# Performance work log

Measured on AMD Instinct MI355X. Metric: run time of the kernel, lower is better.

The kernel has to match this reference:

```python
import jax, jax.numpy as jnp
import numpy as np

EPSILON = 0.01
NITER = 5
EPS_MASS = 1e-9
EPS_LSE = 1e-6


def setup_inputs() -> dict:
    key = jax.random.key(0)
    k1, k2 = jax.random.split(key)
    y = jax.random.uniform(k1, (16, 1, 48, 48), dtype=jnp.float32)
    y_target = jax.random.uniform(k2, (16, 1, 48, 48), dtype=jnp.float32)
    return {"y": y, "y_target": y_target}


def _grid_points(h, w):
    # torch.linspace(0, h-1, h)/h == arange(h)/h
    yg = jnp.arange(h, dtype=jnp.float32) / h
    xg = jnp.arange(w, dtype=jnp.float32) / w
    gy, gx = jnp.meshgrid(yg, xg, indexing="ij")
    return jnp.stack([gy.reshape(-1), gx.reshape(-1)], axis=-1)  # [n, 2]


def reference(y, y_target):
    b, c, h, w = y_target.shape
    g = _grid_points(h, w)                     # [n, 2], same for x and y measures
    # cost_matrix with p=2: sum_k |g_i - g_j|^2 ; grids identical across batch,
    # so compute once as [n, n] and broadcast.
    C = ((g[:, None, :] - g[None, :, :]) ** 2).sum(-1)  # [n, n]

    mass_x = jnp.clip(y.reshape(b, -1), 0.0, 1e9) + EPS_MASS
    mass_y = jnp.clip(y_target.reshape(b, -1), 0.0, 1e9) + EPS_MASS
    mu = mass_x / mass_x.sum(-1, keepdims=True)   # [b, n]
    nu = mass_y / mass_y.sum(-1, keepdims=True)   # [b, n]
    log_mu = jnp.log(mu)
    log_nu = jnp.log(nu)

    def M(u, v):
        # (-C_ij + u_i + v_j) / epsilon, shape [b, n, n]
        return (-C[None, :, :] + u[:, :, None] + v[:, None, :]) / EPSILON

    def lse(A):
        # faithful to original: log(sum(exp(A), axis=2) + 1e-6) (non-shifted)
        return jnp.log(jnp.exp(A).sum(2) + EPS_LSE)

    u = jnp.zeros_like(mu)
    v = jnp.zeros_like(nu)
    for _ in range(NITER):
        u = EPSILON * (log_mu - lse(M(u, v))) + u
        v = EPSILON * (log_nu - lse(jnp.swapaxes(M(u, v), 1, 2))) + v

    pi = jnp.exp(M(u, v))                      # [b, n, n] transport plan
    cost = (pi * C[None, :, :]).sum((1, 2))    # [b]
    return jnp.mean(cost)
```

## Files before the change

kernel.cpp:

```cpp
#include <hip/hip_runtime.h>


#define TPB 576
#define STRIDE 72
#define POISON 0xAAAAAAAAu

typedef __attribute__((ext_vector_type(8))) short short8;
typedef __attribute__((ext_vector_type(4))) short short4v;
typedef __attribute__((ext_vector_type(4))) float f32x4;

__device__ __forceinline__ void splitb(float x, short& hi, short& lo) {
    union { float f; unsigned u; } a, h;
    a.f = x;
    h.u = a.u & 0xffff0000u;
    hi  = (short)(h.u >> 16);
    union { float f; unsigned u; } l;
    l.f = x - h.f;
    lo  = (short)(l.u >> 16);
}

__device__ __forceinline__ short bf16rne(float x) {
    union { float f; unsigned u; } a;
    a.f = x;
    unsigned r = a.u + 0x7fffu + ((a.u >> 16) & 1u);
    return (short)(r >> 16);
}

__device__ __forceinline__ f32x4 mm16(short8 a, short8 b, f32x4 c) {
    return __builtin_amdgcn_mfma_f32_16x16x32_bf16(a, b, c, 0, 0, 0);
}

__global__ __launch_bounds__(TPB) void sinkhorn_kernel(const float* __restrict__ y,
                                                       const float* __restrict__ yt,
                                                       unsigned* __restrict__ parts,
                                                       unsigned* __restrict__ ctr,
                                                       float* __restrict__ out)
{
    __shared__ __align__(16) short sW [48 * STRIDE];
    __shared__ __align__(16) short sP [48 * STRIDE];
    __shared__ __align__(16) short sP2[48 * STRIDE];
    __shared__ float red[32];

    const int t    = threadIdx.x;
    const int b    = blockIdx.x;
    const int lane = t & 63;
    const int wid  = t >> 6;
    const int tr   = wid / 3;
    const int tc   = wid - tr * 3;
    const int n15  = lane & 15;
    const int quad = lane >> 4;
    const int kq   = quad * 8;
    const int r0   = tr * 16 + quad * 4;
    const int c    = tc * 16 + n15;
    const int aBase  = (tr * 16 + n15) * STRIDE;
    const int stBase = c * STRIDE + r0;

    const f32x4 y4  = *(const f32x4*)(y  + b * 2304 + c * 48 + r0);
    const f32x4 yt4 = *(const f32x4*)(yt + b * 2304 + c * 48 + r0);

    short8 Tr0, Tr1;
    short8 Th0, Th1, Tl0, Tl1;
    short8 Dh0, Dh1, Dl0, Dl1;
    {
        const float gm = (float)c / 48.0f;
#pragma unroll
        for (int kk = 0; kk < 8; ++kk) {
            int k0 = kq + kk;
            float d = gm - (float)k0 / 48.0f;
            float dsq = d * d;
            float e = __expf(-100.0f * dsq);
            short h, l;
            Tr0[kk] = bf16rne(e);
            splitb(e, h, l);        Th0[kk] = h; Tl0[kk] = l;
            splitb(e * dsq, h, l);  Dh0[kk] = h; Dl0[kk] = l;
            int k1 = k0 + 32;
            if (k1 < 48) {
                float d1 = gm - (float)k1 / 48.0f;
                float q1 = d1 * d1;
                float e1 = __expf(-100.0f * q1);
                Tr1[kk] = bf16rne(e1);
                splitb(e1, h, l);       Th1[kk] = h; Tl1[kk] = l;
                splitb(e1 * q1, h, l);  Dh1[kk] = h; Dl1[kk] = l;
            } else {
                Tr1[kk] = 0;
                Th1[kk] = 0; Tl1[kk] = 0; Dh1[kk] = 0; Dl1[kk] = 0;
            }
        }
    }

    if (t < 432) {
        const short8 zer  = {0, 0, 0, 0, 0, 0, 0, 0};
        const short  o    = (short)0x3F80;
        const short8 ones = {o, o, o, o, o, o, o, o};
        int ccol = t % 9;
        ((short8*)sW)[t] = (ccol < 6) ? ones : zer;
        if (ccol >= 6) {
            ((short8*)sP )[t] = zer;
            ((short8*)sP2)[t] = zer;
        }
    }

    float mx[4], my[4];
#pragma unroll
    for (int rg = 0; rg < 4; ++rg) {
        mx[rg] = fminf(fmaxf(y4[rg],  0.f), 1e9f) + 1e-9f;
        my[rg] = fminf(fmaxf(yt4[rg], 0.f), 1e9f) + 1e-9f;
    }
    float sx = mx[0] + mx[1] + mx[2] + mx[3];
    float sy = my[0] + my[1] + my[2] + my[3];
#pragma unroll
    for (int off = 32; off > 0; off >>= 1) {
        sx += __shfl_down(sx, off);
        sy += __shfl_down(sy, off);
    }
    if (lane == 0) { red[wid] = sx; red[16 + wid] = sy; }
    __syncthreads();
    float ax = 0.f, ay = 0.f;
#pragma unroll
    for (int w = 0; w < TPB / 64; ++w) { ax += red[w]; ay += red[16 + w]; }
    const float rsx = 1.0f / ax, rsy = 1.0f / ay;

    float mu_[4], nu_[4];
#pragma unroll
    for (int q = 0; q < 4; ++q) { mu_[q] = mx[q] * rsx; nu_[q] = my[q] * rsy; }

    float wu_[4] = {1, 1, 1, 1}, wv_[4] = {1, 1, 1, 1};

    const f32x4 zz = {0.f, 0.f, 0.f, 0.f};

    for (int half = 0; half < 10; ++half) {
        {
            short8 a0 = *(const short8*)(sW + aBase + kq);
            short8 a1 = *(const short8*)(sW + aBase + kq + 32);
            f32x4 x  = mm16(a0, Tr0, zz);
            f32x4 yy = mm16(a1, Tr1, zz);
            f32x4 p = x + yy;
            short4v pk;
#pragma unroll
            for (int rg = 0; rg < 4; ++rg) pk[rg] = bf16rne(p[rg]);
            *(short4v*)(sP + stBase) = pk;
        }
        __syncthreads();
        {
            short8 a0 = *(const short8*)(sP + aBase + kq);
            short8 a1 = *(const short8*)(sP + aBase + kq + 32);
            f32x4 x  = mm16(a0, Tr0, zz);
            f32x4 yy = mm16(a1, Tr1, zz);
            f32x4 S = x + yy;
            float* wc       = ((half & 1) == 0) ? wu_ : wv_;
            const float* m_ = ((half & 1) == 0) ? mu_ : nu_;
            short4v wk;
#pragma unroll
            for (int q = 0; q < 4; ++q) {
                wc[q] = wc[q] * m_[q] / (wc[q] * S[q] + 1e-6f);
                wk[q] = bf16rne(wc[q]);
            }
            *(short4v*)(sW + stBase) = wk;
        }
        __syncthreads();
    }

    {
        short8 a0 = *(const short8*)(sW + aBase + kq);
        short8 a1 = *(const short8*)(sW + aBase + kq + 32);
        f32x4 x1 = mm16(a0, Th0, zz), w1 = mm16(a1, Th1, zz);
        x1 = mm16(a0, Tl0, x1);  w1 = mm16(a1, Tl1, w1);
        f32x4 p1 = x1 + w1;
        f32x4 x2 = mm16(a0, Dh0, zz), w2 = mm16(a1, Dh1, zz);
        x2 = mm16(a0, Dl0, x2);  w2 = mm16(a1, Dl1, w2);
        f32x4 p2 = x2 + w2;
        short4v k1, k2;
#pragma unroll
        for (int rg = 0; rg < 4; ++rg) { k1[rg] = bf16rne(p1[rg]); k2[rg] = bf16rne(p2[rg]); }
        *(short4v*)(sP  + stBase) = k1;
        *(short4v*)(sP2 + stBase) = k2;
    }
    __syncthreads();
    float local;
    {
        short8 a0 = *(const short8*)(sP  + aBase + kq);
        short8 a1 = *(const short8*)(sP  + aBase + kq + 32);
        short8 c0 = *(const short8*)(sP2 + aBase + kq);
        short8 c1 = *(const short8*)(sP2 + aBase + kq + 32);
        f32x4 x  = mm16(a0, Dh0, zz), yy = mm16(a1, Dh1, zz);
        x  = mm16(a0, Dl0, x);   yy = mm16(a1, Dl1, yy);
        x  = mm16(c0, Th0, x);   yy = mm16(c1, Th1, yy);
        x  = mm16(c0, Tl0, x);   yy = mm16(c1, Tl1, yy);
        f32x4 G = x + yy;
        local = wu_[0] * G[0] + wu_[1] * G[1] + wu_[2] * G[2] + wu_[3] * G[3];
    }
#pragma unroll
    for (int off = 32; off > 0; off >>= 1) local += __shfl_down(local, off);
    if (lane == 0) red[wid] = local;
    __syncthreads();

    if (t == 0) {
        float total = 0.f;
#pragma unroll
        for (int w = 0; w < TPB / 64; ++w) total += red[w];
        union { float f; unsigned u; } pu; pu.f = total;
        __hip_atomic_store(&parts[b], pu.u, __ATOMIC_RELEASE,
                           __HIP_MEMORY_SCOPE_AGENT);
        unsigned old = __hip_atomic_fetch_add(ctr, 1u, __ATOMIC_ACQ_REL,
                                              __HIP_MEMORY_SCOPE_AGENT);
        if (old == POISON + 15u) {
            float tot = 0.f;
#pragma unroll
            for (int i = 0; i < 16; ++i) {
                union { unsigned u; float f; } q;
                q.u = __hip_atomic_load(&parts[i], __ATOMIC_RELAXED,
                                        __HIP_MEMORY_SCOPE_AGENT);
                tot += q.f;
            }
            out[0] = tot * (1.0f / 16.0f);
        }
    }
}

extern "C" void kernel_launch(void* const* d_in, const int* in_sizes, int n_in,
                              void* d_out, int out_size, void* d_ws, size_t ws_size,
                              hipStream_t stream)
{
    (void)in_sizes; (void)n_in; (void)ws_size; (void)out_size;
    const float* y  = (const float*)d_in[0];
    const float* yt = (const float*)d_in[1];
    unsigned* parts = (unsigned*)d_ws;
    unsigned* ctr   = (unsigned*)d_ws + 16;
    float*    out   = (float*)d_out;

    sinkhorn_kernel<<<16, TPB, 0, stream>>>(y, yt, parts, ctr, out);
}
```

Baseline: 67.83 us.

## Collapse each batch to a single wavefront with register-shuffle operand exchange

Replaces the 9-wavefront block, which used shared memory and barriers between each separable Gaussian matmul, with one 64-thread wavefront per batch item. Each lane holds a 3x3 grid of MFMA tiles in registers and rebuilds the B operands with cross-lane shuffles, so no LDS or __syncthreads is needed. The kernel matrix is built from shuffles of a 1-D Gaussian table, and the final cost drops the hi/lo bf16 split in favour of single bf16 rounding. The aim is to remove barrier and LDS round-trip latency, in exchange for serial MFMA work on one wave, heavy register use and reduced precision.

```diff
diff --git a/kernel.cpp b/kernel.cpp
--- a/kernel.cpp
+++ b/kernel.cpp
@@ -1,217 +1,294 @@
 #include <hip/hip_runtime.h>
 
 
-#define TPB 576
-#define STRIDE 72
 #define POISON 0xAAAAAAAAu
 
 typedef __attribute__((ext_vector_type(8))) short short8;
-typedef __attribute__((ext_vector_type(4))) short short4v;
 typedef __attribute__((ext_vector_type(4))) float f32x4;
-
-__device__ __forceinline__ void splitb(float x, short& hi, short& lo) {
-    union { float f; unsigned u; } a, h;
-    a.f = x;
-    h.u = a.u & 0xffff0000u;
-    hi  = (short)(h.u >> 16);
-    union { float f; unsigned u; } l;
-    l.f = x - h.f;
-    lo  = (short)(l.u >> 16);
-}
-
-__device__ __forceinline__ short bf16rne(float x) {
-    union { float f; unsigned u; } a;
-    a.f = x;
-    unsigned r = a.u + 0x7fffu + ((a.u >> 16) & 1u);
-    return (short)(r >> 16);
-}
+typedef unsigned int uint;
 
 __device__ __forceinline__ f32x4 mm16(short8 a, short8 b, f32x4 c) {
     return __builtin_amdgcn_mfma_f32_16x16x32_bf16(a, b, c, 0, 0, 0);
 }
-
-__global__ __launch_bounds__(TPB) void sinkhorn_kernel(const float* __restrict__ y,
-                                                       const float* __restrict__ yt,
-                                                       unsigned* __restrict__ parts,
-                                                       unsigned* __restrict__ ctr,
-                                                       float* __restrict__ out)
+__device__ __forceinline__ uint fbits(float x) { union { float f; uint u; } c; c.f = x; return c.u; }
+__device__ __forceinline__ float ffloat(uint x) { union { uint u; float f; } c; c.u = x; return c.f; }
+
+__device__ __forceinline__ uint pack2(float a, float b) {
+    return (fbits(b) & 0xffff0000u) | (fbits(a) >> 16);
+}
+__device__ __forceinline__ float bfr(float x) {
+    uint u = fbits(x);
+    u = (u + 0x7fffu + ((u >> 16) & 1u)) & 0xffff0000u;
+    return ffloat(u);
+}
+__device__ __forceinline__ uint shflu(uint v, int lane) {
+    return (uint)__shfl((int)v, lane, 64);
+}
+
+__device__ __forceinline__ short8 bgather(const uint (&P)[3][3][2], int ch, int cb,
+                                          int addr_a, int addr_b, bool hiq) {
+    uint g0, g1, g2, g3;
+    if (ch == 0) {
+        uint a0 = shflu(P[0][cb][0], addr_a), b0 = shflu(P[1][cb][0], addr_a);
+        uint a1 = shflu(P[0][cb][1], addr_a), b1 = shflu(P[1][cb][1], addr_a);
+        uint a2 = shflu(P[0][cb][0], addr_b), b2 = shflu(P[1][cb][0], addr_b);
+        uint a3 = shflu(P[0][cb][1], addr_b), b3 = shflu(P[1][cb][1], addr_b);
+        g0 = hiq ? b0 : a0; g1 = hiq ? b1 : a1;
+        g2 = hiq ? b2 : a2; g3 = hiq ? b3 : a3;
+    } else {
+        g0 = shflu(P[2][cb][0], addr_a);
+        g1 = shflu(P[2][cb][1], addr_a);
+        g2 = shflu(P[2][cb][0], addr_b);
+        g3 = shflu(P[2][cb][1], addr_b);
+    }
+    union { uint u[4]; short8 s; } cv;
+    cv.u[0] = g0; cv.u[1] = g1; cv.u[2] = g2; cv.u[3] = g3;
+    return cv.s;
+}
+
+__global__ __launch_bounds__(64, 1) void sinkhorn_kernel(const float* __restrict__ y,
+                                                         const float* __restrict__ yt,
+                                                         unsigned* __restrict__ parts,
+                                                         unsigned* __restrict__ ctr,
+                                                         float* __restrict__ out)
 {
-    __shared__ __align__(16) short sW [48 * STRIDE];
-    __shared__ __align__(16) short sP [48 * STRIDE];
-    __shared__ __align__(16) short sP2[48 * STRIDE];
-    __shared__ float red[32];
-
-    const int t    = threadIdx.x;
-    const int b    = blockIdx.x;
-    const int lane = t & 63;
-    const int wid  = t >> 6;
-    const int tr   = wid / 3;
-    const int tc   = wid - tr * 3;
-    const int n15  = lane & 15;
-    const int quad = lane >> 4;
-    const int kq   = quad * 8;
-    const int r0   = tr * 16 + quad * 4;
-    const int c    = tc * 16 + n15;
-    const int aBase  = (tr * 16 + n15) * STRIDE;
-    const int stBase = c * STRIDE + r0;
-
-    const f32x4 y4  = *(const f32x4*)(y  + b * 2304 + c * 48 + r0);
-    const f32x4 yt4 = *(const f32x4*)(yt + b * 2304 + c * 48 + r0);
-
-    short8 Tr0, Tr1;
-    short8 Th0, Th1, Tl0, Tl1;
-    short8 Dh0, Dh1, Dl0, Dl1;
-    {
-        const float gm = (float)c / 48.0f;
-#pragma unroll
-        for (int kk = 0; kk < 8; ++kk) {
-            int k0 = kq + kk;
-            float d = gm - (float)k0 / 48.0f;
-            float dsq = d * d;
-            float e = __expf(-100.0f * dsq);
-            short h, l;
-            Tr0[kk] = bf16rne(e);
-            splitb(e, h, l);        Th0[kk] = h; Tl0[kk] = l;
-            splitb(e * dsq, h, l);  Dh0[kk] = h; Dl0[kk] = l;
-            int k1 = k0 + 32;
-            if (k1 < 48) {
-                float d1 = gm - (float)k1 / 48.0f;
-                float q1 = d1 * d1;
-                float e1 = __expf(-100.0f * q1);
-                Tr1[kk] = bf16rne(e1);
-                splitb(e1, h, l);       Th1[kk] = h; Tl1[kk] = l;
-                splitb(e1 * q1, h, l);  Dh1[kk] = h; Dl1[kk] = l;
-            } else {
-                Tr1[kk] = 0;
-                Th1[kk] = 0; Tl1[kk] = 0; Dh1[kk] = 0; Dl1[kk] = 0;
-            }
-        }
-    }
-
-    if (t < 432) {
-        const short8 zer  = {0, 0, 0, 0, 0, 0, 0, 0};
-        const short  o    = (short)0x3F80;
-        const short8 ones = {o, o, o, o, o, o, o, o};
-        int ccol = t % 9;
-        ((short8*)sW)[t] = (ccol < 6) ? ones : zer;
-        if (ccol >= 6) {
-            ((short8*)sP )[t] = zer;
-            ((short8*)sP2)[t] = zer;
-        }
-    }
-
-    float mx[4], my[4];
-#pragma unroll
-    for (int rg = 0; rg < 4; ++rg) {
-        mx[rg] = fminf(fmaxf(y4[rg],  0.f), 1e9f) + 1e-9f;
-        my[rg] = fminf(fmaxf(yt4[rg], 0.f), 1e9f) + 1e-9f;
-    }
-    float sx = mx[0] + mx[1] + mx[2] + mx[3];
-    float sy = my[0] + my[1] + my[2] + my[3];
-#pragma unroll
-    for (int off = 32; off > 0; off >>= 1) {
-        sx += __shfl_down(sx, off);
-        sy += __shfl_down(sy, off);
-    }
-    if (lane == 0) { red[wid] = sx; red[16 + wid] = sy; }
-    __syncthreads();
-    float ax = 0.f, ay = 0.f;
-#pragma unroll
-    for (int w = 0; w < TPB / 64; ++w) { ax += red[w]; ay += red[16 + w]; }
-    const float rsx = 1.0f / ax, rsy = 1.0f / ay;
-
-    float mu_[4], nu_[4];
-#pragma unroll
-    for (int q = 0; q < 4; ++q) { mu_[q] = mx[q] * rsx; nu_[q] = my[q] * rsy; }
-
-    float wu_[4] = {1, 1, 1, 1}, wv_[4] = {1, 1, 1, 1};
+    const int t = threadIdx.x;
+    const int b = blockIdx.x;
+    const int quad = t >> 4;
+    const int n15  = t & 15;
+    const bool hiq = quad >= 2;
+    const int addr_a = 32 * (quad & 1) + n15;
+    const int addr_b = addr_a + 16;
+
+    f32x4 yv[3][3], ytv[3][3];
+#pragma unroll
+    for (int i = 0; i < 3; ++i)
+#pragma unroll
+        for (int j = 0; j < 3; ++j) {
+            int off = b * 2304 + (j * 16 + n15) * 48 + i * 16 + quad * 4;
+            yv[i][j]  = *(const f32x4*)(y  + off);
+            ytv[i][j] = *(const f32x4*)(yt + off);
+        }
+
+    float dl  = (float)t * (1.0f / 48.0f);
+    float ds2 = dl * dl;
+    float ev  = __expf(-100.0f * ds2);
+    float gv  = bfr(ev);
+    float tdv = bfr(ev * ds2);
+
+    short8 TC[3][2];
+#pragma unroll
+    for (int blk = 0; blk < 3; ++blk)
+#pragma unroll
+        for (int ch = 0; ch < 2; ++ch) {
+            uint w[4];
+#pragma unroll
+            for (int p = 0; p < 4; ++p) {
+                int k0 = ch * 32 + quad * 8 + 2 * p;
+                int r  = blk * 16 + n15;
+                float g0 = __shfl(gv, abs(r - k0), 64);
+                float g1 = __shfl(gv, abs(r - k0 - 1), 64);
+                g0 = (k0     < 48) ? g0 : 0.f;
+                g1 = (k0 + 1 < 48) ? g1 : 0.f;
+                w[p] = pack2(g0, g1);
+            }
+            union { uint u[4]; short8 s; } cv;
+            cv.u[0]=w[0]; cv.u[1]=w[1]; cv.u[2]=w[2]; cv.u[3]=w[3];
+            TC[blk][ch] = cv.s;
+        }
+
+    float mu[3][3][4], nu[3][3][4];
+    float sx = 0.f, sy = 0.f;
+#pragma unroll
+    for (int i = 0; i < 3; ++i)
+#pragma unroll
+        for (int j = 0; j < 3; ++j)
+#pragma unroll
+            for (int rg = 0; rg < 4; ++rg) {
+                float a = fminf(fmaxf(yv[i][j][rg],  0.f), 1e9f) + 1e-9f;
+                float c = fminf(fmaxf(ytv[i][j][rg], 0.f), 1e9f) + 1e-9f;
+                mu[i][j][rg] = a; nu[i][j][rg] = c;
+                sx += a; sy += c;
+            }
+#pragma unroll
+    for (int off = 1; off < 64; off <<= 1) {
+        sx += __shfl_xor(sx, off, 64);
+        sy += __shfl_xor(sy, off, 64);
+    }
+    const float rsx = 1.0f / sx, rsy = 1.0f / sy;
+#pragma unroll
+    for (int i = 0; i < 3; ++i)
+#pragma unroll
+        for (int j = 0; j < 3; ++j)
+#pragma unroll
+            for (int rg = 0; rg < 4; ++rg) { mu[i][j][rg] *= rsx; nu[i][j][rg] *= rsy; }
+
+    float wu[3][3][4], wv[3][3][4];
+    uint Wup[3][3][2], Wvp[3][3][2];
+#pragma unroll
+    for (int i = 0; i < 3; ++i)
+#pragma unroll
+        for (int j = 0; j < 3; ++j) {
+#pragma unroll
+            for (int rg = 0; rg < 4; ++rg) { wu[i][j][rg] = 1.f; wv[i][j][rg] = 1.f; }
+            Wup[i][j][0] = 0x3F803F80u; Wup[i][j][1] = 0x3F803F80u;
+            Wvp[i][j][0] = 0x3F803F80u; Wvp[i][j][1] = 0x3F803F80u;
+        }
 
     const f32x4 zz = {0.f, 0.f, 0.f, 0.f};
 
-    for (int half = 0; half < 10; ++half) {
-        {
-            short8 a0 = *(const short8*)(sW + aBase + kq);
-            short8 a1 = *(const short8*)(sW + aBase + kq + 32);
-            f32x4 x  = mm16(a0, Tr0, zz);
-            f32x4 yy = mm16(a1, Tr1, zz);
-            f32x4 p = x + yy;
-            short4v pk;
-#pragma unroll
-            for (int rg = 0; rg < 4; ++rg) pk[rg] = bf16rne(p[rg]);
-            *(short4v*)(sP + stBase) = pk;
-        }
-        __syncthreads();
-        {
-            short8 a0 = *(const short8*)(sP + aBase + kq);
-            short8 a1 = *(const short8*)(sP + aBase + kq + 32);
-            f32x4 x  = mm16(a0, Tr0, zz);
-            f32x4 yy = mm16(a1, Tr1, zz);
-            f32x4 S = x + yy;
-            float* wc       = ((half & 1) == 0) ? wu_ : wv_;
-            const float* m_ = ((half & 1) == 0) ? mu_ : nu_;
-            short4v wk;
-#pragma unroll
-            for (int q = 0; q < 4; ++q) {
-                wc[q] = wc[q] * m_[q] / (wc[q] * S[q] + 1e-6f);
-                wk[q] = bf16rne(wc[q]);
-            }
-            *(short4v*)(sW + stBase) = wk;
-        }
-        __syncthreads();
-    }
-
-    {
-        short8 a0 = *(const short8*)(sW + aBase + kq);
-        short8 a1 = *(const short8*)(sW + aBase + kq + 32);
-        f32x4 x1 = mm16(a0, Th0, zz), w1 = mm16(a1, Th1, zz);
-        x1 = mm16(a0, Tl0, x1);  w1 = mm16(a1, Tl1, w1);
-        f32x4 p1 = x1 + w1;
-        f32x4 x2 = mm16(a0, Dh0, zz), w2 = mm16(a1, Dh1, zz);
-        x2 = mm16(a0, Dl0, x2);  w2 = mm16(a1, Dl1, w2);
-        f32x4 p2 = x2 + w2;
-        short4v k1, k2;
-#pragma unroll
-        for (int rg = 0; rg < 4; ++rg) { k1[rg] = bf16rne(p1[rg]); k2[rg] = bf16rne(p2[rg]); }
-        *(short4v*)(sP  + stBase) = k1;
-        *(short4v*)(sP2 + stBase) = k2;
-    }
-    __syncthreads();
-    float local;
-    {
-        short8 a0 = *(const short8*)(sP  + aBase + kq);
-        short8 a1 = *(const short8*)(sP  + aBase + kq + 32);
-        short8 c0 = *(const short8*)(sP2 + aBase + kq);
-        short8 c1 = *(const short8*)(sP2 + aBase + kq + 32);
-        f32x4 x  = mm16(a0, Dh0, zz), yy = mm16(a1, Dh1, zz);
-        x  = mm16(a0, Dl0, x);   yy = mm16(a1, Dl1, yy);
-        x  = mm16(c0, Th0, x);   yy = mm16(c1, Th1, yy);
-        x  = mm16(c0, Tl0, x);   yy = mm16(c1, Tl1, yy);
-        f32x4 G = x + yy;
-        local = wu_[0] * G[0] + wu_[1] * G[1] + wu_[2] * G[2] + wu_[3] * G[3];
-    }
-#pragma unroll
-    for (int off = 32; off > 0; off >>= 1) local += __shfl_down(local, off);
-    if (lane == 0) red[wid] = local;
-    __syncthreads();
+    auto half_iter = [&](float (&w)[3][3][4], const float (&m)[3][3][4],
+                         const uint (&srcP)[3][3][2], uint (&dstP)[3][3][2]) {
+        f32x4 Z[3][3];
+#pragma unroll
+        for (int i = 0; i < 3; ++i)
+#pragma unroll
+            for (int j = 0; j < 3; ++j) Z[i][j] = zz;
+#pragma unroll
+        for (int ch = 0; ch < 2; ++ch) {
+            short8 Af[3];
+#pragma unroll
+            for (int cb = 0; cb < 3; ++cb) Af[cb] = bgather(srcP, ch, cb, addr_a, addr_b, hiq);
+#pragma unroll
+            for (int i = 0; i < 3; ++i)
+#pragma unroll
+                for (int j = 0; j < 3; ++j) Z[i][j] = mm16(Af[i], TC[j][ch], Z[i][j]);
+        }
+        uint Zp[3][3][2];
+#pragma unroll
+        for (int i = 0; i < 3; ++i)
+#pragma unroll
+            for (int j = 0; j < 3; ++j) {
+                Zp[i][j][0] = pack2(Z[i][j][0], Z[i][j][1]);
+                Zp[i][j][1] = pack2(Z[i][j][2], Z[i][j][3]);
+            }
+        f32x4 S[3][3];
+#pragma unroll
+        for (int i = 0; i < 3; ++i)
+#pragma unroll
+            for (int j = 0; j < 3; ++j) S[i][j] = zz;
+#pragma unroll
+        for (int ch = 0; ch < 2; ++ch) {
+            short8 Ag[3];
+#pragma unroll
+            for (int cb = 0; cb < 3; ++cb) Ag[cb] = bgather(Zp, ch, cb, addr_a, addr_b, hiq);
+#pragma unroll
+            for (int i = 0; i < 3; ++i)
+#pragma unroll
+                for (int j = 0; j < 3; ++j) S[i][j] = mm16(Ag[i], TC[j][ch], S[i][j]);
+        }
+#pragma unroll
+        for (int i = 0; i < 3; ++i)
+#pragma unroll
+            for (int j = 0; j < 3; ++j) {
+#pragma unroll
+                for (int rg = 0; rg < 4; ++rg) {
+                    float ww = w[i][j][rg];
+                    float dn = fmaf(ww, S[i][j][rg], 1e-6f);
+                    w[i][j][rg] = ww * m[i][j][rg] * __builtin_amdgcn_rcpf(dn);
+                }
+                dstP[i][j][0] = pack2(w[i][j][0], w[i][j][1]);
+                dstP[i][j][1] = pack2(w[i][j][2], w[i][j][3]);
+            }
+    };
+
+    for (int it = 0; it < 5; ++it) {
+        half_iter(wu, mu, Wvp, Wup);
+        half_iter(wv, nu, Wup, Wvp);
+    }
+
+    short8 TD[3][2];
+#pragma unroll
+    for (int blk = 0; blk < 3; ++blk)
+#pragma unroll
+        for (int ch = 0; ch < 2; ++ch) {
+            uint w[4];
+#pragma unroll
+            for (int p = 0; p < 4; ++p) {
+                int k0 = ch * 32 + quad * 8 + 2 * p;
+                int r  = blk * 16 + n15;
+                float g0 = __shfl(tdv, abs(r - k0), 64);
+                float g1 = __shfl(tdv, abs(r - k0 - 1), 64);
+                g0 = (k0     < 48) ? g0 : 0.f;
+                g1 = (k0 + 1 < 48) ? g1 : 0.f;
+                w[p] = pack2(g0, g1);
+            }
+            union { uint u[4]; short8 s; } cv;
+            cv.u[0]=w[0]; cv.u[1]=w[1]; cv.u[2]=w[2]; cv.u[3]=w[3];
+            TD[blk][ch] = cv.s;
+        }
+
+    f32x4 Z1[3][3], Z2[3][3];
+#pragma unroll
+    for (int i = 0; i < 3; ++i)
+#pragma unroll
+        for (int j = 0; j < 3; ++j) { Z1[i][j] = zz; Z2[i][j] = zz; }
+#pragma unroll
+    for (int ch = 0; ch < 2; ++ch) {
+        short8 Af[3];
+#pragma unroll
+        for (int cb = 0; cb < 3; ++cb) Af[cb] = bgather(Wvp, ch, cb, addr_a, addr_b, hiq);
+#pragma unroll
+        for (int i = 0; i < 3; ++i)
+#pragma unroll
+            for (int j = 0; j < 3; ++j) {
+                Z1[i][j] = mm16(Af[i], TC[j][ch], Z1[i][j]);
+                Z2[i][j] = mm16(Af[i], TD[j][ch], Z2[i][j]);
+            }
+    }
+    uint Z1p[3][3][2], Z2p[3][3][2];
+#pragma unroll
+    for (int i = 0; i < 3; ++i)
+#pragma unroll
+        for (int j = 0; j < 3; ++j) {
+            Z1p[i][j][0] = pack2(Z1[i][j][0], Z1[i][j][1]);
+            Z1p[i][j][1] = pack2(Z1[i][j][2], Z1[i][j][3]);
+            Z2p[i][j][0] = pack2(Z2[i][j][0], Z2[i][j][1]);
+            Z2p[i][j][1] = pack2(Z2[i][j][2], Z2[i][j][3]);
+        }
+    f32x4 G[3][3];
+#pragma unroll
+    for (int i = 0; i < 3; ++i)
+#pragma unroll
+        for (int j = 0; j < 3; ++j) G[i][j] = zz;
+#pragma unroll
+    for (int ch = 0; ch < 2; ++ch) {
+        short8 A1[3], A2[3];
+#pragma unroll
+        for (int cb = 0; cb < 3; ++cb) {
+            A1[cb] = bgather(Z1p, ch, cb, addr_a, addr_b, hiq);
+            A2[cb] = bgather(Z2p, ch, cb, addr_a, addr_b, hiq);
+        }
+#pragma unroll
+        for (int i = 0; i < 3; ++i)
+#pragma unroll
+            for (int j = 0; j < 3; ++j) {
+                G[i][j] = mm16(A2[i], TC[j][ch], G[i][j]);
+                G[i][j] = mm16(A1[i], TD[j][ch], G[i][j]);
+            }
+    }
+    float local = 0.f;
+#pragma unroll
+    for (int i = 0; i < 3; ++i)
+#pragma unroll
+        for (int j = 0; j < 3; ++j)
+#pragma unroll
+            for (int rg = 0; rg < 4; ++rg)
+                local = fmaf(wu[i][j][rg], G[i][j][rg], local);
+#pragma unroll
+    for (int off = 32; off > 0; off >>= 1) local += __shfl_down(local, off, 64);
 
     if (t == 0) {
-        float total = 0.f;
-#pragma unroll
-        for (int w = 0; w < TPB / 64; ++w) total += red[w];
-        union { float f; unsigned u; } pu; pu.f = total;
-        __hip_atomic_store(&parts[b], pu.u, __ATOMIC_RELEASE,
+        __hip_atomic_store(&parts[b], fbits(local), __ATOMIC_RELEASE,
                            __HIP_MEMORY_SCOPE_AGENT);
         unsigned old = __hip_atomic_fetch_add(ctr, 1u, __ATOMIC_ACQ_REL,
                                               __HIP_MEMORY_SCOPE_AGENT);
         if (old == POISON + 15u) {
             float tot = 0.f;
 #pragma unroll
-            for (int i = 0; i < 16; ++i) {
-                union { unsigned u; float f; } q;
-                q.u = __hip_atomic_load(&parts[i], __ATOMIC_RELAXED,
-                                        __HIP_MEMORY_SCOPE_AGENT);
-                tot += q.f;
-            }
+            for (int i = 0; i < 16; ++i)
+                tot += ffloat(__hip_atomic_load(&parts[i], __ATOMIC_RELAXED,
+                                                __HIP_MEMORY_SCOPE_AGENT));
             out[0] = tot * (1.0f / 16.0f);
         }
     }
@@ -228,5 +305,5 @@
     unsigned* ctr   = (unsigned*)d_ws + 16;
     float*    out   = (float*)d_out;
 
-    sinkhorn_kernel<<<16, TPB, 0, stream>>>(y, yt, parts, ctr, out);
-}
+    sinkhorn_kernel<<<16, 64, 0, stream>>>(y, yt, parts, ctr, out);
+}
```

After: 69.88 us. 1.03x slower.
